# Kernel optimization log

Hardware: AMD Instinct MI355X
Metric: run time of the kernel (lower is better)

Reference implementation:

```python
import jax, jax.numpy as jnp
import numpy as np

S, D, H, F = 4096, 2048, 16, 8192
HD = D // H
EPS = 1e-5


def setup_inputs() -> dict:
    key = jax.random.key(0)
    ks = jax.random.split(key, 16)
    sc_d = 1.0 / np.sqrt(D)
    sc_f = 1.0 / np.sqrt(F)
    return {
        "x": jax.random.normal(ks[0], (S, D), dtype=jnp.float32),
        # stacked per-head projections: [H, D, HD]
        "Wq": jax.random.normal(ks[1], (H, D, HD), dtype=jnp.float32) * sc_d,
        "bq": jax.random.normal(ks[2], (H, HD), dtype=jnp.float32) * 0.01,
        "Wk": jax.random.normal(ks[3], (H, D, HD), dtype=jnp.float32) * sc_d,
        "bk": jax.random.normal(ks[4], (H, HD), dtype=jnp.float32) * 0.01,
        "Wv": jax.random.normal(ks[5], (H, D, HD), dtype=jnp.float32) * sc_d,
        "bv": jax.random.normal(ks[6], (H, HD), dtype=jnp.float32) * 0.01,
        "Wp": jax.random.normal(ks[7], (D, D), dtype=jnp.float32) * sc_d,
        "bp": jax.random.normal(ks[8], (D,), dtype=jnp.float32) * 0.01,
        "W1": jax.random.normal(ks[9], (D, F), dtype=jnp.float32) * sc_d,
        "b1": jax.random.normal(ks[10], (F,), dtype=jnp.float32) * 0.01,
        "W2": jax.random.normal(ks[11], (F, D), dtype=jnp.float32) * sc_f,
        "b2": jax.random.normal(ks[12], (D,), dtype=jnp.float32) * 0.01,
        "gamma": jnp.ones((D,), dtype=jnp.float32),
        "beta": jnp.zeros((D,), dtype=jnp.float32),
    }


def _layernorm(x, gamma, beta):
    mu = jnp.mean(x, axis=-1, keepdims=True)
    var = jnp.var(x, axis=-1, keepdims=True)
    return (x - mu) * jax.lax.rsqrt(var + EPS) * gamma + beta


def reference(x, Wq, bq, Wk, bk, Wv, bv, Wp, bp, W1, b1, W2, b2, gamma, beta):
    residual = x
    # batched per-head projections: [H, S, HD]
    q = jnp.einsum('sd,hde->hse', x, Wq) + bq[:, None, :]
    k = jnp.einsum('sd,hde->hse', x, Wk) + bk[:, None, :]
    v = jnp.einsum('sd,hde->hse', x, Wv) + bv[:, None, :]
    scores = jnp.einsum('hse,hte->hst', q, k) / np.sqrt(HD).astype(np.float32)
    attn = jax.nn.softmax(scores, axis=-1)
    heads = jnp.einsum('hst,hte->hse', attn, v)  # [H, S, HD]
    # concat heads along feature dim (head 0 first): [S, H*HD]
    heads = jnp.transpose(heads, (1, 0, 2)).reshape(S, H * HD)
    out = heads @ Wp + bp
    # residual_attn=True, norm_attn=True
    out = out + residual
    out = _layernorm(out, gamma, beta)
    # feedforward (original forward ends here)
    out = jax.nn.relu(out @ W1 + b1) @ W2 + b2
    return out
```

## Files before the change

kernel.cpp:

```cpp
#include <hip/hip_runtime.h>
#include <hip/hip_bf16.h>
#include <cstdint>
#include <cstddef>

#define S 4096
#define D 2048
#define H 16
#define HD 128
#define F 8192

typedef unsigned short ushort_t;
typedef __attribute__((ext_vector_type(8))) short short8;
typedef __attribute__((ext_vector_type(4))) float floatx4;

__device__ __forceinline__ ushort_t f2bf(float f) {
  union { float f; unsigned u; } v; v.f = f;
  unsigned u = v.u;
  return (ushort_t)((u + 0x7fffu + ((u >> 16) & 1u)) >> 16);
}

__device__ __forceinline__ void async16(void* lds, const void* g) {
  __builtin_amdgcn_global_load_lds(
      (const __attribute__((address_space(1))) unsigned int*)g,
      (__attribute__((address_space(3))) unsigned int*)lds, 16, 0, 0);
}


__global__ void cast_bf16(const float* __restrict__ src, ushort_t* __restrict__ dst, int n4) {
  int i = blockIdx.x * blockDim.x + threadIdx.x;
  if (i < n4) {
    float4 v = ((const float4*)src)[i];
    ushort4 o;
    o.x = f2bf(v.x); o.y = f2bf(v.y); o.z = f2bf(v.z); o.w = f2bf(v.w);
    ((ushort4*)dst)[i] = o;
  }
}

__global__ void build_bqkv(const float* __restrict__ bq, const float* __restrict__ bk,
                           const float* __restrict__ bv, float* __restrict__ bqkv) {
  int n = blockIdx.x * blockDim.x + threadIdx.x;
  if (n < 3 * D) {
    float v;
    if (n < D) v = bq[n];
    else if (n < 2 * D) v = bk[n - D];
    else v = bv[n - 2 * D];
    bqkv[n] = v;
  }
}

__global__ void transpose_f32_bf16(const float* __restrict__ src, ushort_t* __restrict__ dst,
                                   int ldS, int ldD, long srcBatchStride, long dstBatchRows) {
  __shared__ float t[32][33];
  int b = blockIdx.z;
  src += (size_t)b * srcBatchStride;
  dst += (size_t)b * dstBatchRows * ldD;
  int r0 = blockIdx.x * 32, c0 = blockIdx.y * 32;
  int tx = threadIdx.x, ty = threadIdx.y;
#pragma unroll
  for (int i = 0; i < 4; ++i)
    t[ty + i * 8][tx] = src[(size_t)(r0 + ty + i * 8) * ldS + c0 + tx];
  __syncthreads();
#pragma unroll
  for (int i = 0; i < 4; ++i)
    dst[(size_t)(c0 + ty + i * 8) * ldD + r0 + tx] = f2bf(t[tx][ty + i * 8]);
}

__global__ void transpose_bf16(const ushort_t* __restrict__ src, ushort_t* __restrict__ dst,
                               int ldS, int ldD, int colOff) {
  __shared__ ushort_t t[32][33];
  int r0 = blockIdx.x * 32, c0 = blockIdx.y * 32;
  int tx = threadIdx.x, ty = threadIdx.y;
#pragma unroll
  for (int i = 0; i < 4; ++i)
    t[ty + i * 8][tx] = src[(size_t)(r0 + ty + i * 8) * ldS + colOff + c0 + tx];
  __syncthreads();
#pragma unroll
  for (int i = 0; i < 4; ++i)
    dst[(size_t)(c0 + ty + i * 8) * ldD + r0 + tx] = t[tx][ty + i * 8];
}

template <int MODE>
__global__ __launch_bounds__(256, 2)
void gemm_bt(const ushort_t* __restrict__ A, const ushort_t* __restrict__ Bt,
             const float* __restrict__ bias, const float* __restrict__ resid,
             ushort_t* __restrict__ outb, float* __restrict__ outf,
             int M, int N, int K) {
  __shared__ __align__(16) ushort_t As[128 * 32];
  __shared__ __align__(16) ushort_t Bs[128 * 32];
  const int tid = threadIdx.x;
  const int w = tid >> 6, l = tid & 63;
  const int wr = w >> 1, wc = w & 1;
  const int g = l >> 4, c16 = l & 15;
  const int m0 = blockIdx.y * 128, n0 = blockIdx.x * 128;

  floatx4 acc[4][4];
#pragma unroll
  for (int i = 0; i < 4; ++i)
#pragma unroll
    for (int j = 0; j < 4; ++j) acc[i][j] = (floatx4){0.f, 0.f, 0.f, 0.f};

  for (int k0 = 0; k0 < K; k0 += 32) {
#pragma unroll
    for (int c = 0; c < 2; ++c) {
      int flat = (c * 256 + tid) * 16;
      int row = flat >> 6, colb = flat & 63;
      const char* ga = (const char*)A + ((size_t)(m0 + row) * K + k0) * 2 + colb;
      async16((char*)As + (size_t)(c * 256 + w * 64) * 16, ga);
      const char* gb = (const char*)Bt + ((size_t)(n0 + row) * K + k0) * 2 + colb;
      async16((char*)Bs + (size_t)(c * 256 + w * 64) * 16, gb);
    }
    __syncthreads();
    short8 af[4], bf[4];
#pragma unroll
    for (int i = 0; i < 4; ++i)
      af[i] = *(const short8*)(As + (wr * 64 + i * 16 + c16) * 32 + g * 8);
#pragma unroll
    for (int j = 0; j < 4; ++j)
      bf[j] = *(const short8*)(Bs + (wc * 64 + j * 16 + c16) * 32 + g * 8);
#pragma unroll
    for (int i = 0; i < 4; ++i)
#pragma unroll
      for (int j = 0; j < 4; ++j)
        acc[i][j] = __builtin_amdgcn_mfma_f32_16x16x32_bf16(af[i], bf[j], acc[i][j], 0, 0, 0);
    __syncthreads();
  }

#pragma unroll
  for (int j = 0; j < 4; ++j) {
    int gcol = n0 + wc * 64 + j * 16 + c16;
    float bj = bias[gcol];
#pragma unroll
    for (int i = 0; i < 4; ++i) {
      int rbase = m0 + wr * 64 + i * 16 + g * 4;
#pragma unroll
      for (int r = 0; r < 4; ++r) {
        int grow = rbase + r;
        float v = acc[i][j][r] + bj;
        if (MODE == 0) {
          outb[(size_t)grow * N + gcol] = f2bf(v);
        } else if (MODE == 1) {
          outf[(size_t)grow * N + gcol] = v + resid[(size_t)grow * N + gcol];
        } else if (MODE == 2) {
          outb[(size_t)grow * N + gcol] = f2bf(v > 0.f ? v : 0.f);
        } else {
          outf[(size_t)grow * N + gcol] = v;
        }
      }
    }
  }
}

__global__ __launch_bounds__(256, 2)
void attn_kernel(const ushort_t* __restrict__ QKV, const ushort_t* __restrict__ Vt,
                 ushort_t* __restrict__ heads) {
  const int h = blockIdx.y;
  const int tid = threadIdx.x, w = tid >> 6, l = tid & 63;
  const int g = l >> 4, c = l & 15;
  const int q0 = blockIdx.x * 128 + w * 32;
  const float scale = 0.08838834764831845f;

  __shared__ __align__(16) ushort_t Ks[64 * 128];
  __shared__ __align__(16) ushort_t Vs[128 * 64];
  __shared__ __align__(16) ushort_t Ps[4][2][16][72];

  short8 qf[2][4];
#pragma unroll
  for (int u = 0; u < 2; ++u)
#pragma unroll
    for (int k0 = 0; k0 < 4; ++k0)
      qf[u][k0] = *(const short8*)(QKV + (size_t)(q0 + u * 16 + c) * (3 * D) + h * HD + k0 * 32 + g * 8);

  floatx4 o[2][8];
#pragma unroll
  for (int u = 0; u < 2; ++u)
#pragma unroll
    for (int j = 0; j < 8; ++j) o[u][j] = (floatx4){0.f, 0.f, 0.f, 0.f};
  float l_run[2] = {0.f, 0.f};

  for (int t0 = 0; t0 < S; t0 += 64) {
#pragma unroll
    for (int cc = 0; cc < 4; ++cc) {
      int slot = cc * 256 + tid;
      int krow = slot >> 4, kch = slot & 15;
      const char* gk = (const char*)QKV +
          ((size_t)(t0 + krow) * (3 * D) + D + h * HD) * 2 + ((kch ^ (krow & 15)) << 4);
      async16((char*)Ks + (size_t)(cc * 256 + w * 64) * 16, gk);
      int vrow = slot >> 3, vch = slot & 7;
      const char* gv = (const char*)Vt +
          ((size_t)(h * HD + vrow) * S + t0) * 2 + ((vch ^ (vrow & 7)) << 4);
      async16((char*)Vs + (size_t)(cc * 256 + w * 64) * 16, gv);
    }
    __syncthreads();

    floatx4 sc[2][4];
#pragma unroll
    for (int u = 0; u < 2; ++u)
#pragma unroll
      for (int tt = 0; tt < 4; ++tt) sc[u][tt] = (floatx4){0.f, 0.f, 0.f, 0.f};
#pragma unroll
    for (int tt = 0; tt < 4; ++tt) {
      short8 kf[4];
#pragma unroll
      for (int k0 = 0; k0 < 4; ++k0)
        kf[k0] = *(const short8*)(Ks + (tt * 16 + c) * 128 + (((k0 * 4 + g) ^ c) << 3));
#pragma unroll
      for (int u = 0; u < 2; ++u)
#pragma unroll
        for (int k0 = 0; k0 < 4; ++k0)
          sc[u][tt] = __builtin_amdgcn_mfma_f32_16x16x32_bf16(kf[k0], qf[u][k0], sc[u][tt], 0, 0, 0);
    }

#pragma unroll
    for (int u = 0; u < 2; ++u) {
#pragma unroll
      for (int tt = 0; tt < 4; ++tt) {
        float p0 = __expf(sc[u][tt][0] * scale);
        float p1 = __expf(sc[u][tt][1] * scale);
        float p2 = __expf(sc[u][tt][2] * scale);
        float p3 = __expf(sc[u][tt][3] * scale);
        l_run[u] += p0 + p1 + p2 + p3;
        ushort4 pk;
        pk.x = f2bf(p0); pk.y = f2bf(p1); pk.z = f2bf(p2); pk.w = f2bf(p3);
        *reinterpret_cast<ushort4*>(&Ps[w][u][c][tt * 16 + g * 4]) = pk;
      }
    }
    __asm__ volatile("s_waitcnt lgkmcnt(0)" ::: "memory");

    short8 pf[2][2];
#pragma unroll
    for (int u = 0; u < 2; ++u)
#pragma unroll
      for (int tk = 0; tk < 2; ++tk)
        pf[u][tk] = *reinterpret_cast<const short8*>(&Ps[w][u][c][tk * 32 + g * 8]);
#pragma unroll
    for (int j = 0; j < 8; ++j) {
#pragma unroll
      for (int tk = 0; tk < 2; ++tk) {
        short8 vf = *(const short8*)(Vs + (j * 16 + c) * 64 + (((tk * 4 + g) ^ (c & 7)) << 3));
#pragma unroll
        for (int u = 0; u < 2; ++u)
          o[u][j] = __builtin_amdgcn_mfma_f32_16x16x32_bf16(pf[u][tk], vf, o[u][j], 0, 0, 0);
      }
    }
    __syncthreads();
  }

#pragma unroll
  for (int u = 0; u < 2; ++u) {
    float lt = l_run[u];
    lt += __shfl_xor(lt, 16);
    lt += __shfl_xor(lt, 32);
    float linv[4];
#pragma unroll
    for (int r = 0; r < 4; ++r) linv[r] = 1.f / __shfl(lt, g * 4 + r);
    ushort_t* hp = heads + (size_t)(q0 + u * 16 + g * 4) * D + h * HD + c;
#pragma unroll
    for (int j = 0; j < 8; ++j)
#pragma unroll
      for (int r = 0; r < 4; ++r)
        hp[(size_t)r * D + j * 16] = f2bf(o[u][j][r] * linv[r]);
  }
}

__global__ __launch_bounds__(256)
void ln_kernel(const float* __restrict__ preln, const float* __restrict__ gamma,
               const float* __restrict__ beta, ushort_t* __restrict__ y) {
  int row = blockIdx.x, tid = threadIdx.x;
  const float* p = preln + (size_t)row * D;
  float vals[8];
  float sum = 0.f, ss = 0.f;
#pragma unroll
  for (int k = 0; k < 8; ++k) {
    float v = p[tid + k * 256];
    vals[k] = v; sum += v; ss += v * v;
  }
#pragma unroll
  for (int off = 32; off >= 1; off >>= 1) {
    sum += __shfl_xor(sum, off);
    ss += __shfl_xor(ss, off);
  }
  __shared__ float s1[4], s2[4];
  int w = tid >> 6, l = tid & 63;
  if (l == 0) { s1[w] = sum; s2[w] = ss; }
  __syncthreads();
  sum = s1[0] + s1[1] + s1[2] + s1[3];
  ss = s2[0] + s2[1] + s2[2] + s2[3];
  float mu = sum / (float)D;
  float var = ss / (float)D - mu * mu;
  float rs = rsqrtf(var + 1e-5f);
  ushort_t* yr = y + (size_t)row * D;
#pragma unroll
  for (int k = 0; k < 8; ++k) {
    int d = tid + k * 256;
    yr[d] = f2bf((vals[k] - mu) * rs * gamma[d] + beta[d]);
  }
}


extern "C" void kernel_launch(void* const* d_in, const int* in_sizes, int n_in,
                              void* d_out, int out_size, void* d_ws, size_t ws_size,
                              hipStream_t stream) {
  const float* x = (const float*)d_in[0];
  const float* Wq = (const float*)d_in[1];
  const float* bq = (const float*)d_in[2];
  const float* Wk = (const float*)d_in[3];
  const float* bk = (const float*)d_in[4];
  const float* Wv = (const float*)d_in[5];
  const float* bv = (const float*)d_in[6];
  const float* Wp = (const float*)d_in[7];
  const float* bp = (const float*)d_in[8];
  const float* W1 = (const float*)d_in[9];
  const float* b1 = (const float*)d_in[10];
  const float* W2 = (const float*)d_in[11];
  const float* b2 = (const float*)d_in[12];
  const float* gamma = (const float*)d_in[13];
  const float* beta = (const float*)d_in[14];

  char* ws = (char*)d_ws;
  ushort_t* WQKVT = (ushort_t*)(ws + 0);
  ushort_t* XB    = (ushort_t*)(ws + 25165824);
  float*    BQKV  = (float*)(ws + 41943040);
  ushort_t* WPT   = (ushort_t*)(ws + 41975808);
  ushort_t* W1T   = (ushort_t*)(ws + 50364416);
  ushort_t* W2T   = (ushort_t*)(ws + 83918848);
  ushort_t* QKV   = (ushort_t*)(ws + 117473280);
  ushort_t* HEADS = (ushort_t*)(ws + 167804928);
  ushort_t* VT    = (ushort_t*)(ws + 184582144);
  float*    PRELN = (float*)(ws + 0);
  ushort_t* AB    = (ushort_t*)(ws + 117473280);
  ushort_t* Y     = (ushort_t*)(ws + 184582144);
  float* OUT = (float*)d_out;

  dim3 tb(32, 8);
  cast_bf16<<<(S * D / 4 + 255) / 256, 256, 0, stream>>>(x, XB, S * D / 4);
  build_bqkv<<<(3 * D + 255) / 256, 256, 0, stream>>>(bq, bk, bv, BQKV);
  transpose_f32_bf16<<<dim3(D / 32, HD / 32, H), tb, 0, stream>>>(Wq, WQKVT, HD, D, (long)D * HD, HD);
  transpose_f32_bf16<<<dim3(D / 32, HD / 32, H), tb, 0, stream>>>(Wk, WQKVT + (size_t)D * D, HD, D, (long)D * HD, HD);
  transpose_f32_bf16<<<dim3(D / 32, HD / 32, H), tb, 0, stream>>>(Wv, WQKVT + (size_t)2 * D * D, HD, D, (long)D * HD, HD);
  transpose_f32_bf16<<<dim3(D / 32, D / 32, 1), tb, 0, stream>>>(Wp, WPT, D, D, 0, 0);
  transpose_f32_bf16<<<dim3(D / 32, F / 32, 1), tb, 0, stream>>>(W1, W1T, F, D, 0, 0);
  transpose_f32_bf16<<<dim3(F / 32, D / 32, 1), tb, 0, stream>>>(W2, W2T, D, F, 0, 0);
  gemm_bt<0><<<dim3(3 * D / 128, S / 128), 256, 0, stream>>>(XB, WQKVT, BQKV, nullptr, QKV, nullptr, S, 3 * D, D);
  transpose_bf16<<<dim3(S / 32, D / 32), tb, 0, stream>>>(QKV, VT, 3 * D, S, 2 * D);
  attn_kernel<<<dim3(S / 128, H), 256, 0, stream>>>(QKV, VT, HEADS);
  gemm_bt<1><<<dim3(D / 128, S / 128), 256, 0, stream>>>(HEADS, WPT, bp, x, nullptr, PRELN, S, D, D);
  ln_kernel<<<S, 256, 0, stream>>>(PRELN, gamma, beta, Y);
  gemm_bt<2><<<dim3(F / 128, S / 128), 256, 0, stream>>>(Y, W1T, b1, nullptr, AB, nullptr, S, F, D);
  gemm_bt<3><<<dim3(D / 128, S / 128), 256, 0, stream>>>(AB, W2T, b2, nullptr, nullptr, OUT, S, D, F);
}
```

Baseline: 1.020 ms.

## Add split-K with atomics and grouped tile ordering to GEMMs

Switches the GEMM grid to a 1-D launch with grouped (8-row super-tile) block ordering for better L2 reuse of B tiles. Adds a split-K template parameter; the out-projection and W2 GEMMs split K in two and accumulate into zeroed fp32 outputs with atomicAdd, giving the under-filled 512-block grids more blocks. In exchange it adds memsets, atomic traffic on the fp32 outputs and non-deterministic summation order.

```diff
diff --git a/kernel.cpp b/kernel.cpp
--- a/kernel.cpp
+++ b/kernel.cpp
@@ -79,7 +79,7 @@
     dst[(size_t)(c0 + ty + i * 8) * ldD + r0 + tx] = t[tx][ty + i * 8];
 }
 
-template <int MODE>
+template <int MODE, int SPLITK>
 __global__ __launch_bounds__(256, 2)
 void gemm_bt(const ushort_t* __restrict__ A, const ushort_t* __restrict__ Bt,
              const float* __restrict__ bias, const float* __restrict__ resid,
@@ -91,7 +91,20 @@
   const int w = tid >> 6, l = tid & 63;
   const int wr = w >> 1, wc = w & 1;
   const int g = l >> 4, c16 = l & 15;
-  const int m0 = blockIdx.y * 128, n0 = blockIdx.x * 128;
+
+  const int tilesM = M >> 7, tilesN = N >> 7;
+  int pid = blockIdx.x;
+  int ks = 0;
+  if (SPLITK > 1) {
+    ks = pid / (tilesM * tilesN);
+    pid -= ks * (tilesM * tilesN);
+  }
+  const int npg = 8 * tilesN;
+  const int gid = pid / npg;
+  const int pm = gid * 8 + (pid & 7);
+  const int pn = (pid % npg) >> 3;
+  const int m0 = pm * 128, n0 = pn * 128;
+  const int kLen = K / SPLITK, kStart = ks * kLen;
 
   floatx4 acc[4][4];
 #pragma unroll
@@ -99,7 +112,7 @@
 #pragma unroll
     for (int j = 0; j < 4; ++j) acc[i][j] = (floatx4){0.f, 0.f, 0.f, 0.f};
 
-  for (int k0 = 0; k0 < K; k0 += 32) {
+  for (int k0 = kStart; k0 < kStart + kLen; k0 += 32) {
 #pragma unroll
     for (int c = 0; c < 2; ++c) {
       int flat = (c * 256 + tid) * 16;
@@ -128,22 +141,26 @@
 #pragma unroll
   for (int j = 0; j < 4; ++j) {
     int gcol = n0 + wc * 64 + j * 16 + c16;
-    float bj = bias[gcol];
+    float bj = (SPLITK == 1 || ks == 0) ? bias[gcol] : 0.f;
 #pragma unroll
     for (int i = 0; i < 4; ++i) {
       int rbase = m0 + wr * 64 + i * 16 + g * 4;
 #pragma unroll
       for (int r = 0; r < 4; ++r) {
         int grow = rbase + r;
+        size_t idx = (size_t)grow * N + gcol;
         float v = acc[i][j][r] + bj;
-        if (MODE == 0) {
-          outb[(size_t)grow * N + gcol] = f2bf(v);
+        if (SPLITK > 1) {
+          if (MODE == 1 && ks == 0) v += resid[idx];
+          atomicAdd(&outf[idx], v);
+        } else if (MODE == 0) {
+          outb[idx] = f2bf(v);
         } else if (MODE == 1) {
-          outf[(size_t)grow * N + gcol] = v + resid[(size_t)grow * N + gcol];
+          outf[idx] = v + resid[idx];
         } else if (MODE == 2) {
-          outb[(size_t)grow * N + gcol] = f2bf(v > 0.f ? v : 0.f);
+          outb[idx] = f2bf(v > 0.f ? v : 0.f);
         } else {
-          outf[(size_t)grow * N + gcol] = v;
+          outf[idx] = v;
         }
       }
     }
@@ -332,6 +349,7 @@
   float* OUT = (float*)d_out;
 
   dim3 tb(32, 8);
+  hipMemsetAsync(d_out, 0, (size_t)out_size * 4, stream);
   cast_bf16<<<(S * D / 4 + 255) / 256, 256, 0, stream>>>(x, XB, S * D / 4);
   build_bqkv<<<(3 * D + 255) / 256, 256, 0, stream>>>(bq, bk, bv, BQKV);
   transpose_f32_bf16<<<dim3(D / 32, HD / 32, H), tb, 0, stream>>>(Wq, WQKVT, HD, D, (long)D * HD, HD);
@@ -340,11 +358,16 @@
   transpose_f32_bf16<<<dim3(D / 32, D / 32, 1), tb, 0, stream>>>(Wp, WPT, D, D, 0, 0);
   transpose_f32_bf16<<<dim3(D / 32, F / 32, 1), tb, 0, stream>>>(W1, W1T, F, D, 0, 0);
   transpose_f32_bf16<<<dim3(F / 32, D / 32, 1), tb, 0, stream>>>(W2, W2T, D, F, 0, 0);
-  gemm_bt<0><<<dim3(3 * D / 128, S / 128), 256, 0, stream>>>(XB, WQKVT, BQKV, nullptr, QKV, nullptr, S, 3 * D, D);
+  gemm_bt<0, 1><<<(S / 128) * (3 * D / 128), 256, 0, stream>>>(
+      XB, WQKVT, BQKV, nullptr, QKV, nullptr, S, 3 * D, D);
+  hipMemsetAsync(PRELN, 0, (size_t)S * D * 4, stream);
   transpose_bf16<<<dim3(S / 32, D / 32), tb, 0, stream>>>(QKV, VT, 3 * D, S, 2 * D);
   attn_kernel<<<dim3(S / 128, H), 256, 0, stream>>>(QKV, VT, HEADS);
-  gemm_bt<1><<<dim3(D / 128, S / 128), 256, 0, stream>>>(HEADS, WPT, bp, x, nullptr, PRELN, S, D, D);
+  gemm_bt<1, 2><<<(S / 128) * (D / 128) * 2, 256, 0, stream>>>(
+      HEADS, WPT, bp, x, nullptr, PRELN, S, D, D);
   ln_kernel<<<S, 256, 0, stream>>>(PRELN, gamma, beta, Y);
-  gemm_bt<2><<<dim3(F / 128, S / 128), 256, 0, stream>>>(Y, W1T, b1, nullptr, AB, nullptr, S, F, D);
-  gemm_bt<3><<<dim3(D / 128, S / 128), 256, 0, stream>>>(AB, W2T, b2, nullptr, nullptr, OUT, S, D, F);
-}
+  gemm_bt<2, 1><<<(S / 128) * (F / 128), 256, 0, stream>>>(
+      Y, W1T, b1, nullptr, AB, nullptr, S, F, D);
+  gemm_bt<3, 2><<<(S / 128) * (D / 128) * 2, 256, 0, stream>>>(
+      AB, W2T, b2, nullptr, nullptr, OUT, S, D, F);
+}
```

Measured after the change: 1.064 ms. 4.3% more time.
